# Kernel tuning notes

Measured on AMD Instinct MI355X. Metric: run time of the kernel, lower is better.

Reference implementation:

```python
import jax, jax.numpy as jnp
import numpy as np

MARGIN = 6.0
EPSILON = 2.0
REL_DIM = 256
REL_RANGE = (MARGIN + EPSILON) / REL_DIM  # OpenKE rel_embedding_range = 0.03125
PI = 3.14159265358979323846


def setup_inputs() -> dict:
    key = jax.random.key(0)
    k1, k2, k3, k4, k5 = jax.random.split(key, 5)
    B, S, H = 16, 64, 768
    E, D2 = 43234, 512  # entity count, entity embed dim (2*256)
    return {
        "question_hidden": jax.random.normal(k1, (B, S, H), dtype=jnp.float32),
        "W_rel": jax.random.normal(k2, (18, H), dtype=jnp.float32) * 0.02,
        "b_rel": jnp.zeros((18,), dtype=jnp.float32),
        "rel_embeddings": jax.random.normal(k3, (18, REL_DIM), dtype=jnp.float32) * REL_RANGE,
        "ent_embeddings": jax.random.normal(k4, (E, D2), dtype=jnp.float32) * 0.05,
        "head_id": jax.random.randint(k5, (B,), 0, E, dtype=jnp.int64),
    }


def reference(question_hidden, W_rel, b_rel, rel_embeddings, ent_embeddings, head_id):
    # RelationPredictor: mean-pool BERT hidden states, then Linear(768 -> 18)
    q = jnp.mean(question_hidden, axis=1)                       # (B, 768)
    rel_scores = q @ W_rel.T + b_rel                            # (B, 18)
    # soft relation mixture -> predicted relation embedding
    predict_relation = jax.nn.sigmoid(rel_scores) @ rel_embeddings  # (B, 256)
    head = ent_embeddings[head_id]                              # (B, 512)
    re_h, im_h = jnp.split(head, 2, axis=-1)                    # (B, 256) each
    phase = predict_relation / (REL_RANGE / PI)
    re_r, im_r = jnp.cos(phase), jnp.sin(phase)
    # rotate head by relation (complex multiply)
    rot_re = re_h * re_r - im_h * im_r                          # (B, 256)
    rot_im = re_h * im_r + im_h * re_r                          # (B, 256)
    re_t, im_t = jnp.split(ent_embeddings, 2, axis=-1)          # (E, 256) each
    # broadcast distance vs all entities: (B, E, 256) intermediates
    dre = rot_re[:, None, :] - re_t[None, :, :]
    dim_ = rot_im[:, None, :] - im_t[None, :, :]
    dist = jnp.sqrt(dre * dre + dim_ * dim_).sum(axis=-1)       # (B, E)
    return MARGIN - dist
```

## Files before the change

### kernel.cpp

```cpp
#include <hip/hip_runtime.h>
#include <hip/hip_bf16.h>
#include <math.h>

#define MARGIN_F 6.0f
#define PHASE_SCALE 100.53096491487338f

__global__ void k_prep(const float* __restrict__ qh, const float* __restrict__ W,
                       const float* __restrict__ brel,
                       const float* __restrict__ rel,
                       const float* __restrict__ ent, const int* __restrict__ hid,
                       float* __restrict__ rot) {
    __shared__ float q[768];
    __shared__ float sig[18];
    int b = blockIdx.x;
    int t = threadIdx.x;

    if (t < 768) {
        float s = 0.f;
        const float* base = qh + (size_t)b * 64 * 768 + t;
        #pragma unroll 8
        for (int srow = 0; srow < 64; ++srow) s += base[(size_t)srow * 768];
        q[t] = s * (1.0f / 64.0f);
    }
    __syncthreads();

    int wave = t >> 6, lane = t & 63;
    for (int r = wave; r < 18; r += 16) {
        float p = 0.f;
        for (int h = lane; h < 768; h += 64) p += q[h] * W[r * 768 + h];
        for (int off = 32; off; off >>= 1) p += __shfl_xor(p, off, 64);
        if (lane == 0) sig[r] = 1.0f / (1.0f + expf(-(p + brel[r])));
    }
    __syncthreads();

    if (t < 256) {
        int d = t;
        float pr = 0.f;
        #pragma unroll
        for (int r = 0; r < 18; ++r) pr += sig[r] * rel[r * 256 + d];
        float phase = pr * PHASE_SCALE;
        float sn, cs;
        sincosf(phase, &sn, &cs);
        int h0 = hid[b];
        float reh = ent[(size_t)h0 * 512 + d];
        float imh = ent[(size_t)h0 * 512 + 256 + d];
        rot[b * 256 + d]        = reh * cs - imh * sn;
        rot[4096 + b * 256 + d] = reh * sn + imh * cs;
    }
}

__global__ __launch_bounds__(256, 4) void k_dist(const float* __restrict__ ent,
                                                 const float* __restrict__ rot,
                                                 float* __restrict__ out, int E,
                                                 int chunk) {
    int lane = threadIdx.x & 63;
    int wid = blockIdx.x * 4 + (threadIdx.x >> 6);
    int bhalf = wid & 1;
    int pair = wid >> 1;

    const float4* rre4 = (const float4*)rot + (size_t)bhalf * 8 * 64;
    const float4* rim4 = (const float4*)(rot + 4096) + (size_t)bhalf * 8 * 64;

    int bout = bhalf * 8 + (((lane & 1) << 2) | (lane & 2) | ((lane >> 2) & 1));

    int e0 = (int)((long long)pair * chunk);
    int e1 = min(e0 + chunk, E);
    if (e0 >= e1) return;

    for (int e = e0; e < e1; ++e) {
        const float4* r4 = (const float4*)(ent + (size_t)e * 512);
        float4 te = r4[lane];
        float4 ti = r4[64 + lane];

        float v[8];
        #pragma unroll
        for (int b = 0; b < 8; ++b) {
            float4 rr = rre4[b * 64 + lane];
            float4 ri = rim4[b * 64 + lane];
            float dx0 = rr.x - te.x, dy0 = ri.x - ti.x;
            float dx1 = rr.y - te.y, dy1 = ri.y - ti.y;
            float dx2 = rr.z - te.z, dy2 = ri.z - ti.z;
            float dx3 = rr.w - te.w, dy3 = ri.w - ti.w;
            float s0 = __builtin_amdgcn_sqrtf(dx0 * dx0 + dy0 * dy0);
            float s1 = __builtin_amdgcn_sqrtf(dx1 * dx1 + dy1 * dy1);
            float s2 = __builtin_amdgcn_sqrtf(dx2 * dx2 + dy2 * dy2);
            float s3 = __builtin_amdgcn_sqrtf(dx3 * dx3 + dy3 * dy3);
            v[b] = (s0 + s1) + (s2 + s3);
        }

        #pragma unroll
        for (int i = 0; i < 4; ++i) {
            float send = (lane & 1) ? v[i] : v[i + 4];
            float recv = __shfl_xor(send, 1, 64);
            v[i] = ((lane & 1) ? v[i + 4] : v[i]) + recv;
        }
        #pragma unroll
        for (int i = 0; i < 2; ++i) {
            float send = (lane & 2) ? v[i] : v[i + 2];
            float recv = __shfl_xor(send, 2, 64);
            v[i] = ((lane & 2) ? v[i + 2] : v[i]) + recv;
        }
        {
            float send = (lane & 4) ? v[0] : v[1];
            float recv = __shfl_xor(send, 4, 64);
            v[0] = ((lane & 4) ? v[1] : v[0]) + recv;
        }
        v[0] += __shfl_xor(v[0], 8, 64);
        v[0] += __shfl_xor(v[0], 16, 64);
        v[0] += __shfl_xor(v[0], 32, 64);

        if (lane < 8) out[(size_t)bout * E + e] = MARGIN_F - v[0];
    }
}

extern "C" void kernel_launch(void* const* d_in, const int* in_sizes, int n_in,
                              void* d_out, int out_size, void* d_ws,
                              size_t ws_size, hipStream_t stream) {
    const float* qh   = (const float*)d_in[0];
    const float* W    = (const float*)d_in[1];
    const float* brel = (const float*)d_in[2];
    const float* rel  = (const float*)d_in[3];
    const float* ent  = (const float*)d_in[4];
    const int*   hid  = (const int*)d_in[5];
    float* out = (float*)d_out;

    int E = in_sizes[4] / 512;

    float* rot = (float*)d_ws;

    k_prep<<<dim3(16), 1024, 0, stream>>>(qh, W, brel, rel, ent, hid, rot);

    const int NB = 2048;
    int npairs = NB * 4 / 2;
    int chunk = (E + npairs - 1) / npairs;
    k_dist<<<dim3(NB), 256, 0, stream>>>(ent, rot, out, E, chunk);
}
```

Before: 57.43 us.

## Split batch across four waves per block and keep rotated heads in registers

Each block now handles one entity chunk, and each of its four waves covers four batch rows instead of two waves covering eight rows each. Every wave loads its four rotated-head vectors into registers once, so the inner loop no longer reloads them for every entity. Each entity row is now read by four waves rather than two, relying on L1/L2 to absorb the repeat reads. The shuffle reduction is shorter, and register pressure is lower than an eight-row register cache would need.

```diff
diff --git a/kernel.cpp b/kernel.cpp
--- a/kernel.cpp
+++ b/kernel.cpp
@@ -54,33 +54,34 @@
                                                  float* __restrict__ out, int E,
                                                  int chunk) {
     int lane = threadIdx.x & 63;
-    int wid = blockIdx.x * 4 + (threadIdx.x >> 6);
-    int bhalf = wid & 1;
-    int pair = wid >> 1;
+    int w4 = threadIdx.x >> 6;
 
-    const float4* rre4 = (const float4*)rot + (size_t)bhalf * 8 * 64;
-    const float4* rim4 = (const float4*)(rot + 4096) + (size_t)bhalf * 8 * 64;
+    const float4* rre4 = (const float4*)rot + (size_t)w4 * 4 * 64;
+    const float4* rim4 = (const float4*)(rot + 4096) + (size_t)w4 * 4 * 64;
+    float4 ra[4], ia[4];
+    #pragma unroll
+    for (int b = 0; b < 4; ++b) {
+        ra[b] = rre4[b * 64 + lane];
+        ia[b] = rim4[b * 64 + lane];
+    }
 
-    int bout = bhalf * 8 + (((lane & 1) << 2) | (lane & 2) | ((lane >> 2) & 1));
+    int bout = w4 * 4 + (((lane & 1) << 1) | ((lane >> 1) & 1));
 
-    int e0 = (int)((long long)pair * chunk);
+    int e0 = blockIdx.x * chunk;
     int e1 = min(e0 + chunk, E);
-    if (e0 >= e1) return;
 
     for (int e = e0; e < e1; ++e) {
         const float4* r4 = (const float4*)(ent + (size_t)e * 512);
         float4 te = r4[lane];
         float4 ti = r4[64 + lane];
 
-        float v[8];
+        float v[4];
         #pragma unroll
-        for (int b = 0; b < 8; ++b) {
-            float4 rr = rre4[b * 64 + lane];
-            float4 ri = rim4[b * 64 + lane];
-            float dx0 = rr.x - te.x, dy0 = ri.x - ti.x;
-            float dx1 = rr.y - te.y, dy1 = ri.y - ti.y;
-            float dx2 = rr.z - te.z, dy2 = ri.z - ti.z;
-            float dx3 = rr.w - te.w, dy3 = ri.w - ti.w;
+        for (int b = 0; b < 4; ++b) {
+            float dx0 = ra[b].x - te.x, dy0 = ia[b].x - ti.x;
+            float dx1 = ra[b].y - te.y, dy1 = ia[b].y - ti.y;
+            float dx2 = ra[b].z - te.z, dy2 = ia[b].z - ti.z;
+            float dx3 = ra[b].w - te.w, dy3 = ia[b].w - ti.w;
             float s0 = __builtin_amdgcn_sqrtf(dx0 * dx0 + dy0 * dy0);
             float s1 = __builtin_amdgcn_sqrtf(dx1 * dx1 + dy1 * dy1);
             float s2 = __builtin_amdgcn_sqrtf(dx2 * dx2 + dy2 * dy2);
@@ -89,27 +90,22 @@
         }
 
         #pragma unroll
-        for (int i = 0; i < 4; ++i) {
-            float send = (lane & 1) ? v[i] : v[i + 4];
+        for (int i = 0; i < 2; ++i) {
+            float send = (lane & 1) ? v[i] : v[i + 2];
             float recv = __shfl_xor(send, 1, 64);
-            v[i] = ((lane & 1) ? v[i + 4] : v[i]) + recv;
-        }
-        #pragma unroll
-        for (int i = 0; i < 2; ++i) {
-            float send = (lane & 2) ? v[i] : v[i + 2];
-            float recv = __shfl_xor(send, 2, 64);
-            v[i] = ((lane & 2) ? v[i + 2] : v[i]) + recv;
+            v[i] = ((lane & 1) ? v[i + 2] : v[i]) + recv;
         }
         {
-            float send = (lane & 4) ? v[0] : v[1];
-            float recv = __shfl_xor(send, 4, 64);
-            v[0] = ((lane & 4) ? v[1] : v[0]) + recv;
+            float send = (lane & 2) ? v[0] : v[1];
+            float recv = __shfl_xor(send, 2, 64);
+            v[0] = ((lane & 2) ? v[1] : v[0]) + recv;
         }
+        v[0] += __shfl_xor(v[0], 4, 64);
         v[0] += __shfl_xor(v[0], 8, 64);
         v[0] += __shfl_xor(v[0], 16, 64);
         v[0] += __shfl_xor(v[0], 32, 64);
 
-        if (lane < 8) out[(size_t)bout * E + e] = MARGIN_F - v[0];
+        if (lane < 4) out[(size_t)bout * E + e] = MARGIN_F - v[0];
     }
 }
 
@@ -131,7 +127,6 @@
     k_prep<<<dim3(16), 1024, 0, stream>>>(qh, W, brel, rel, ent, hid, rot);
 
     const int NB = 2048;
-    int npairs = NB * 4 / 2;
-    int chunk = (E + npairs - 1) / npairs;
+    int chunk = (E + NB - 1) / NB;
     k_dist<<<dim3(NB), 256, 0, stream>>>(ent, rot, out, E, chunk);
 }
```

After: 57.25 us. Within noise of the previous version (-0.3%).
